# Kernel optimization log

Measured on AMD Instinct MI355X. Metric: run time of the kernel, lower is better.

## Reference

```python
import jax, jax.numpy as jnp
import numpy as np

N, E, DEG, DIM, NFP, NSEQ = 8192, 65536, 16, 64, 10000, 1024
LGNN, RAD, LOUT, NCLS = 3, 2, 2, 2


def setup_inputs() -> dict:
    key = jax.random.key(0)
    ks = jax.random.split(key, 24)
    s = 0.02
    return {
        "fingerprints": jax.random.randint(ks[0], (N,), 0, NFP + 1),
        "atom_degree_list": jax.random.randint(ks[1], (N, DEG), 0, N),
        "bond_feature": jax.random.normal(ks[2], (E, 10), jnp.float32),
        "bond_degree_list": jax.random.randint(ks[3], (N, DEG), 0, E),
        "i_bond_j": jax.random.randint(ks[4], (E, 2), 0, N),
        # scale down so adjacency @ hs does not saturate the sigmoids
        "adjacency": jax.random.uniform(ks[5], (N, N), jnp.float32) * (1.0 / 128.0),
        "words": jax.random.normal(ks[6], (NSEQ,), jnp.float32),
        "embed_table": jax.random.normal(ks[7], (NFP + 1, DIM), jnp.float32) * s,
        "bond_W": jax.random.normal(ks[8], (10, DIM), jnp.float32) * s,
        "bond_b": jnp.zeros((DIM,), jnp.float32),
        "sub_W": jax.random.normal(ks[9], (RAD, DIM, DIM), jnp.float32) * s,
        "sub_b": jnp.zeros((RAD, DIM), jnp.float32),
        "neigh_W": jax.random.normal(ks[10], (LGNN, 2 * DIM, DIM), jnp.float32) * s,
        "neigh_b": jnp.zeros((LGNN, DIM), jnp.float32),
        "side_W": jax.random.normal(ks[11], (LGNN, DIM, DIM), jnp.float32) * s,
        "side_b": jnp.zeros((LGNN, DIM), jnp.float32),
        "fc_W": jax.random.uniform(ks[12], (NSEQ, DIM), jnp.float32, -0.01, 0.01),
        "fc_b": jnp.zeros((DIM,), jnp.float32),
        "out_W": jax.random.normal(ks[13], (LOUT, 2 * DIM, 2 * DIM), jnp.float32) * s,
        "out_b": jnp.zeros((LOUT, 2 * DIM), jnp.float32),
        "inter_W": jax.random.normal(ks[14], (2 * DIM, NCLS), jnp.float32) * s,
        "inter_b": jnp.zeros((NCLS,), jnp.float32),
    }


def reference(fingerprints, atom_degree_list, bond_feature, bond_degree_list,
              i_bond_j, adjacency, words, embed_table, bond_W, bond_b,
              sub_W, sub_b, neigh_W, neigh_b, side_W, side_b,
              fc_W, fc_b, out_W, out_b, inter_W, inter_b):
    # sub_graph: residual dense-adjacency propagation
    x = embed_table[fingerprints]                       # [N, dim]
    for i in range(RAD):
        hs = jax.nn.relu(x @ sub_W[i] + sub_b[i])
        x = x + adjacency @ hs

    # gnn: gather neighbors, concat, linear+leaky_relu, sum, sigmoid updates
    bond_f = bond_feature @ bond_W + bond_b             # [E, dim]
    atom_f = x
    for i in range(LGNN):
        bn = bond_f[bond_degree_list]                   # [N, DEG, dim]
        an = atom_f[atom_degree_list]                   # [N, DEG, dim]
        nf = jnp.concatenate([an, bn], axis=-1)         # [N, DEG, 2*dim]
        nf = jax.nn.leaky_relu(nf @ neigh_W[i] + neigh_b[i], 0.01)
        atom_f = jax.nn.sigmoid(atom_f + nf.sum(axis=-2))
        pair = atom_f[i_bond_j].sum(axis=-2)            # [E, dim]
        bond_f = jax.nn.sigmoid(bond_f + pair @ side_W[i] + side_b[i])

    disease_vector = jnp.mean(x + atom_f, axis=0)[None, :]   # [1, dim]

    # miRNA vector via MLP
    mirna_vector = words.reshape(1, -1) @ fc_W + fc_b        # [1, dim]

    cat = jnp.concatenate([disease_vector, mirna_vector], axis=1)  # [1, 2*dim]
    for j in range(LOUT):
        cat = jax.nn.relu(cat @ out_W[j] + out_b[j])
    association = cat @ inter_W + inter_b                    # [1, n_classes]
    return association
```

## Files before the change

kernel.cpp:

```cpp
#include <hip/hip_runtime.h>
#include <hip/hip_bf16.h>
#include <cstdint>
#include <cstddef>

#define N_ATOM 8192
#define N_EDGE 65536
#define DEG    16
#define DIM    64
#define ADJ_S  4
#define BM     64
#define BK     64

typedef __attribute__((ext_vector_type(8))) short bf16x8_t;
typedef __attribute__((ext_vector_type(4))) float f32x4_t;

__device__ __forceinline__ float sigmoidf_(float z) {
  return 1.0f / (1.0f + __expf(-z));
}
__device__ __forceinline__ float lrelu_(float z) {
  return z > 0.0f ? z : 0.01f * z;
}
__device__ __forceinline__ unsigned short f2bfu(float f) {
  union { __hip_bfloat16 h; unsigned short u; } v;
  v.h = __float2bfloat16(f);
  return v.u;
}
__device__ __forceinline__ float bf2f(unsigned short u) {
  union { unsigned int i; float f; } v;
  v.i = ((unsigned int)u) << 16;
  return v.f;
}
__device__ __forceinline__ float4 cvt4f(ushort4 u) {
  return make_float4(bf2f(u.x), bf2f(u.y), bf2f(u.z), bf2f(u.w));
}
__device__ __forceinline__ ushort4 cvt4b(float4 f) {
  ushort4 u;
  u.x = f2bfu(f.x); u.y = f2bfu(f.y); u.z = f2bfu(f.z); u.w = f2bfu(f.w);
  return u;
}
__device__ __forceinline__ bf16x8_t cvt8(const float4 a, const float4 b) {
  bf16x8_t r;
  r[0] = (short)f2bfu(a.x); r[1] = (short)f2bfu(a.y);
  r[2] = (short)f2bfu(a.z); r[3] = (short)f2bfu(a.w);
  r[4] = (short)f2bfu(b.x); r[5] = (short)f2bfu(b.y);
  r[6] = (short)f2bfu(b.z); r[7] = (short)f2bfu(b.w);
  return r;
}
__device__ __forceinline__ void gload16(const void* g, void* l) {
  __builtin_amdgcn_global_load_lds(
      (const __attribute__((address_space(1))) void*)g,
      (__attribute__((address_space(3))) void*)l, 16, 0, 0);
}

__global__ __launch_bounds__(256) void k_front(
    const int* __restrict__ fp, const float* __restrict__ emb,
    float* __restrict__ x, const float* __restrict__ W,
    const float* __restrict__ b, unsigned short* __restrict__ hsT,
    const float* __restrict__ bfeat, const float* __restrict__ bW,
    const float* __restrict__ bb, unsigned short* __restrict__ bond_bf,
    const float* __restrict__ Wbn0, unsigned short* __restrict__ B_bf,
    const float* __restrict__ words, const float* __restrict__ fcW,
    float* __restrict__ mp2) {
  __shared__ float xs[16][68];
  __shared__ float Ws[64][64];
  const int t = threadIdx.x;
  const int r = t >> 4, dq = t & 15, d0 = dq * 4;
  if (blockIdx.x < (N_ATOM / 16)) {
    const int row = blockIdx.x * 16 + r;
    float4 v = reinterpret_cast<const float4*>(emb)[(size_t)fp[row] * 16 + dq];
    reinterpret_cast<float4*>(x)[(size_t)row * 16 + dq] = v;
    *reinterpret_cast<float4*>(&xs[r][d0]) = v;
#pragma unroll
    for (int q = 0; q < 4; ++q) {
      int p = t + q * 256;
      reinterpret_cast<float4*>(&Ws[0][0])[p] =
          reinterpret_cast<const float4*>(W)[p];
    }
    __syncthreads();
    float4 acc = reinterpret_cast<const float4*>(b)[dq];
#pragma unroll
    for (int k = 0; k < 64; ++k) {
      float xv = xs[r][k];
      float4 wv = *reinterpret_cast<const float4*>(&Ws[k][d0]);
      acc.x = fmaf(xv, wv.x, acc.x);
      acc.y = fmaf(xv, wv.y, acc.y);
      acc.z = fmaf(xv, wv.z, acc.z);
      acc.w = fmaf(xv, wv.w, acc.w);
    }
    float a4[4] = {acc.x, acc.y, acc.z, acc.w};
#pragma unroll
    for (int j = 0; j < 4; ++j)
      hsT[(size_t)(d0 + j) * N_ATOM + row] = f2bfu(fmaxf(a4[j], 0.0f));
  } else if (blockIdx.x < (N_ATOM / 16 + N_EDGE / 16)) {
    const int row = (blockIdx.x - N_ATOM / 16) * 16 + r;
    float4 acc = reinterpret_cast<const float4*>(bb)[dq];
    const float* br = bfeat + (size_t)row * 10;
#pragma unroll
    for (int k = 0; k < 10; ++k) {
      float xv = br[k];
      float4 wv = reinterpret_cast<const float4*>(bW)[k * 16 + dq];
      acc.x = fmaf(xv, wv.x, acc.x);
      acc.y = fmaf(xv, wv.y, acc.y);
      acc.z = fmaf(xv, wv.z, acc.z);
      acc.w = fmaf(xv, wv.w, acc.w);
    }
    reinterpret_cast<ushort4*>(bond_bf)[(size_t)row * 16 + dq] = cvt4b(acc);
    *reinterpret_cast<float4*>(&xs[r][d0]) = acc;
#pragma unroll
    for (int q = 0; q < 4; ++q) {
      int p = t + q * 256;
      reinterpret_cast<float4*>(&Ws[0][0])[p] =
          reinterpret_cast<const float4*>(Wbn0)[p];
    }
    __syncthreads();
    float4 acc2 = make_float4(0.f, 0.f, 0.f, 0.f);
#pragma unroll
    for (int k = 0; k < 64; ++k) {
      float xv = xs[r][k];
      float4 wv = *reinterpret_cast<const float4*>(&Ws[k][d0]);
      acc2.x = fmaf(xv, wv.x, acc2.x);
      acc2.y = fmaf(xv, wv.y, acc2.y);
      acc2.z = fmaf(xv, wv.z, acc2.z);
      acc2.w = fmaf(xv, wv.w, acc2.w);
    }
    reinterpret_cast<ushort4*>(B_bf)[(size_t)row * 16 + dq] = cvt4b(acc2);
  } else {
    const int mb = blockIdx.x - (N_ATOM / 16 + N_EDGE / 16);
    const int k = mb * 16 + r;
    float wv = words[k];
    float4 fv = reinterpret_cast<const float4*>(fcW)[(size_t)k * 16 + dq];
    float4 acc = make_float4(wv * fv.x, wv * fv.y, wv * fv.z, wv * fv.w);
    float4* red4 = reinterpret_cast<float4*>(&Ws[0][0]);
    red4[t] = acc;
    __syncthreads();
    for (int h = 8; h >= 1; h >>= 1) {
      if (r < h) {
        float4 o = red4[t + h * 16];
        acc.x += o.x; acc.y += o.y; acc.z += o.z; acc.w += o.w;
        red4[t] = acc;
      }
      __syncthreads();
    }
    if (r == 0) reinterpret_cast<float4*>(mp2)[mb * 16 + dq] = acc;
  }
}

__global__ __launch_bounds__(256) void k_red_hs(
    const float* __restrict__ part, float* __restrict__ x,
    const float* __restrict__ W, const float* __restrict__ b,
    unsigned short* __restrict__ hsT) {
  __shared__ float xs[16][68];
  __shared__ float Ws[64][64];
  const int t = threadIdx.x;
  const int r = t >> 4, dq = t & 15, d0 = dq * 4;
  const int row = blockIdx.x * 16 + r;
  float4 v = reinterpret_cast<const float4*>(x)[(size_t)row * 16 + dq];
#pragma unroll
  for (int s = 0; s < ADJ_S; ++s) {
    float4 p = reinterpret_cast<const float4*>(part)
                   [(size_t)s * (N_ATOM * 16) + (size_t)row * 16 + dq];
    v.x += p.x; v.y += p.y; v.z += p.z; v.w += p.w;
  }
  reinterpret_cast<float4*>(x)[(size_t)row * 16 + dq] = v;
  *reinterpret_cast<float4*>(&xs[r][d0]) = v;
#pragma unroll
  for (int q = 0; q < 4; ++q) {
    int p = t + q * 256;
    reinterpret_cast<float4*>(&Ws[0][0])[p] =
        reinterpret_cast<const float4*>(W)[p];
  }
  __syncthreads();
  float4 acc = reinterpret_cast<const float4*>(b)[dq];
#pragma unroll
  for (int k = 0; k < 64; ++k) {
    float xv = xs[r][k];
    float4 wv = *reinterpret_cast<const float4*>(&Ws[k][d0]);
    acc.x = fmaf(xv, wv.x, acc.x);
    acc.y = fmaf(xv, wv.y, acc.y);
    acc.z = fmaf(xv, wv.z, acc.z);
    acc.w = fmaf(xv, wv.w, acc.w);
  }
  float a4[4] = {acc.x, acc.y, acc.z, acc.w};
#pragma unroll
  for (int j = 0; j < 4; ++j)
    hsT[(size_t)(d0 + j) * N_ATOM + row] = f2bfu(fmaxf(a4[j], 0.0f));
}

__global__ __launch_bounds__(256) void k_adjmm(
    const float* __restrict__ adj, const unsigned short* __restrict__ hsT,
    float* __restrict__ part) {
  __shared__ float          Abuf[2][BM * BK];
  __shared__ unsigned short Bbuf[2][64 * BK];
  const int t = threadIdx.x;
  const int lane = t & 63, w = t >> 6;
  const int lr = lane & 15, lg = lane >> 4;
  const int row0 = blockIdx.x * BM;
  const int kbase = blockIdx.y * (N_ATOM / ADJ_S);
  const int NSTEP = (N_ATOM / ADJ_S) / BK;

  size_t aSrc[4]; int aLds[4];
#pragma unroll
  for (int j = 0; j < 4; ++j) {
    int c = j * 256 + t;
    int row = c >> 4, u = c & 15;
    int us = (u & 8) | ((u & 7) ^ (row & 7));
    aSrc[j] = (size_t)(row0 + row) * N_ATOM + kbase + us * 4;
    aLds[j] = j * 1024 + w * 256;
  }
  size_t bSrc[2]; int bLds[2];
#pragma unroll
  for (int j = 0; j < 2; ++j) {
    int c = j * 256 + t;
    int row = c >> 3, u = c & 7;
    int us = u ^ (row & 7);
    bSrc[j] = (size_t)row * N_ATOM + kbase + us * 8;
    bLds[j] = j * 2048 + w * 512;
  }

  f32x4_t acc[4];
#pragma unroll
  for (int n = 0; n < 4; ++n) acc[n] = (f32x4_t){0.f, 0.f, 0.f, 0.f};

#define STAGE(buf, kt)                                                        \
  {                                                                           \
    _Pragma("unroll")                                                         \
    for (int j = 0; j < 4; ++j)                                               \
      gload16(adj + aSrc[j] + (kt) * BK, &Abuf[buf][aLds[j]]);                \
    _Pragma("unroll")                                                         \
    for (int j = 0; j < 2; ++j)                                               \
      gload16(hsT + bSrc[j] + (kt) * BK, &Bbuf[buf][bLds[j]]);                \
  }

  STAGE(0, 0);
  __syncthreads();
  int cur = 0;
  const int Rl = w * 16 + lr;
  for (int kt = 0; kt < NSTEP; ++kt) {
    if (kt + 1 < NSTEP) STAGE(cur ^ 1, kt + 1);
#pragma unroll
    for (int kf = 0; kf < 2; ++kf) {
      int ua = kf * 8 + ((2 * lg) ^ (Rl & 7));
      int ub = kf * 8 + ((2 * lg + 1) ^ (Rl & 7));
      float4 fa = *reinterpret_cast<const float4*>(&Abuf[cur][Rl * 64 + ua * 4]);
      float4 fb = *reinterpret_cast<const float4*>(&Abuf[cur][Rl * 64 + ub * 4]);
      bf16x8_t a = cvt8(fa, fb);
#pragma unroll
      for (int n = 0; n < 4; ++n) {
        int Rb = n * 16 + lr;
        int us = (kf * 4 + lg) ^ (Rb & 7);
        bf16x8_t bv = *reinterpret_cast<const bf16x8_t*>(&Bbuf[cur][Rb * 64 + us * 8]);
        acc[n] = __builtin_amdgcn_mfma_f32_16x16x32_bf16(a, bv, acc[n], 0, 0, 0);
      }
    }
    __syncthreads();
    cur ^= 1;
  }
#undef STAGE

  float* pp = part + (size_t)blockIdx.y * (N_ATOM * DIM);
#pragma unroll
  for (int n = 0; n < 4; ++n)
#pragma unroll
    for (int rg = 0; rg < 4; ++rg) {
      int row = row0 + w * 16 + lg * 4 + rg;
      int col = n * 16 + lr;
      pp[(size_t)row * DIM + col] = acc[n][rg];
    }
}

__global__ __launch_bounds__(256) void k_A0(
    float* __restrict__ atom_f, const float* __restrict__ nW0,
    const float* __restrict__ nb0, unsigned short* __restrict__ A,
    const float* __restrict__ part, float* __restrict__ x) {
  __shared__ float xs[16][68];
  __shared__ float Ws[64][64];
  int t = threadIdx.x;
  int r = t >> 4, dq = t & 15, d0 = dq * 4;
  int row = blockIdx.x * 16 + r;
  float4 v = reinterpret_cast<const float4*>(x)[(size_t)row * 16 + dq];
#pragma unroll
  for (int s = 0; s < ADJ_S; ++s) {
    float4 p = reinterpret_cast<const float4*>(part)
                   [(size_t)s * (N_ATOM * 16) + (size_t)row * 16 + dq];
    v.x += p.x; v.y += p.y; v.z += p.z; v.w += p.w;
  }
  reinterpret_cast<float4*>(x)[(size_t)row * 16 + dq] = v;
  reinterpret_cast<float4*>(atom_f)[(size_t)row * 16 + dq] = v;
  *reinterpret_cast<float4*>(&xs[r][d0]) = v;
#pragma unroll
  for (int q = 0; q < 4; ++q) {
    int p = t + q * 256;
    reinterpret_cast<float4*>(&Ws[0][0])[p] = reinterpret_cast<const float4*>(nW0)[p];
  }
  __syncthreads();
  float4 acc = reinterpret_cast<const float4*>(nb0)[dq];
#pragma unroll
  for (int k = 0; k < 64; ++k) {
    float xv = xs[r][k];
    float4 wv = *reinterpret_cast<const float4*>(&Ws[k][d0]);
    acc.x = fmaf(xv, wv.x, acc.x);
    acc.y = fmaf(xv, wv.y, acc.y);
    acc.z = fmaf(xv, wv.z, acc.z);
    acc.w = fmaf(xv, wv.w, acc.w);
  }
  reinterpret_cast<ushort4*>(A)[(size_t)row * 16 + dq] = cvt4b(acc);
}

__global__ __launch_bounds__(256) void k_upd(
    const int* __restrict__ adl, const int* __restrict__ bdl,
    const unsigned short* __restrict__ A, const unsigned short* __restrict__ B,
    float* __restrict__ atom_f, const float* __restrict__ WanN,
    const float* __restrict__ nbN, unsigned short* __restrict__ A_next,
    const float* __restrict__ x, float* __restrict__ mp, int has_next) {
  __shared__ float xs[16][68];
  __shared__ float Ws[64][64];
  int t = threadIdx.x;
  int r = t >> 4, dq = t & 15, d0 = dq * 4;
  int n = blockIdx.x * 16 + r;
  float4 s = make_float4(0.f, 0.f, 0.f, 0.f);
#pragma unroll
  for (int g = 0; g < DEG; ++g) {
    int ai = adl[n * DEG + g];
    int bi = bdl[n * DEG + g];
    float4 va = cvt4f(reinterpret_cast<const ushort4*>(A)[(size_t)ai * 16 + dq]);
    float4 vb = cvt4f(reinterpret_cast<const ushort4*>(B)[(size_t)bi * 16 + dq]);
    s.x += lrelu_(va.x + vb.x);
    s.y += lrelu_(va.y + vb.y);
    s.z += lrelu_(va.z + vb.z);
    s.w += lrelu_(va.w + vb.w);
  }
  float4 af = reinterpret_cast<const float4*>(atom_f)[(size_t)n * 16 + dq];
  af.x = sigmoidf_(af.x + s.x);
  af.y = sigmoidf_(af.y + s.y);
  af.z = sigmoidf_(af.z + s.z);
  af.w = sigmoidf_(af.w + s.w);
  reinterpret_cast<float4*>(atom_f)[(size_t)n * 16 + dq] = af;
  if (has_next) {
    *reinterpret_cast<float4*>(&xs[r][d0]) = af;
#pragma unroll
    for (int q = 0; q < 4; ++q) {
      int p = t + q * 256;
      reinterpret_cast<float4*>(&Ws[0][0])[p] =
          reinterpret_cast<const float4*>(WanN)[p];
    }
    __syncthreads();
    float4 acc = reinterpret_cast<const float4*>(nbN)[dq];
#pragma unroll
    for (int k = 0; k < 64; ++k) {
      float xv = xs[r][k];
      float4 wv = *reinterpret_cast<const float4*>(&Ws[k][d0]);
      acc.x = fmaf(xv, wv.x, acc.x);
      acc.y = fmaf(xv, wv.y, acc.y);
      acc.z = fmaf(xv, wv.z, acc.z);
      acc.w = fmaf(xv, wv.w, acc.w);
    }
    reinterpret_cast<ushort4*>(A_next)[(size_t)n * 16 + dq] = cvt4b(acc);
  } else {
    float4 xv = reinterpret_cast<const float4*>(x)[(size_t)n * 16 + dq];
    float4 c = make_float4(af.x + xv.x, af.y + xv.y, af.z + xv.z, af.w + xv.w);
    float4* red4 = reinterpret_cast<float4*>(&Ws[0][0]);
    red4[t] = c;
    __syncthreads();
    for (int h = 8; h >= 1; h >>= 1) {
      if (r < h) {
        float4 o = red4[t + h * 16];
        c.x += o.x; c.y += o.y; c.z += o.z; c.w += o.w;
        red4[t] = c;
      }
      __syncthreads();
    }
    if (r == 0) reinterpret_cast<float4*>(mp)[blockIdx.x * 16 + dq] = c;
  }
}

__global__ __launch_bounds__(256) void k_side(
    const int* __restrict__ ibj, const float* __restrict__ atom_f,
    const float* __restrict__ sW, const float* __restrict__ sb,
    unsigned short* __restrict__ bond_bf, const float* __restrict__ WbnN,
    unsigned short* __restrict__ B_next, int write_bond) {
  __shared__ float ps[16][68];
  __shared__ float Ws[64][64];
  int t = threadIdx.x;
  int r = t >> 4, dq = t & 15, d0 = dq * 4;
  int e = blockIdx.x * 16 + r;
  int i0 = ibj[e * 2], i1 = ibj[e * 2 + 1];
  float4 p0 = reinterpret_cast<const float4*>(atom_f)[(size_t)i0 * 16 + dq];
  float4 p1 = reinterpret_cast<const float4*>(atom_f)[(size_t)i1 * 16 + dq];
  float4 pv = make_float4(p0.x + p1.x, p0.y + p1.y, p0.z + p1.z, p0.w + p1.w);
  *reinterpret_cast<float4*>(&ps[r][d0]) = pv;
#pragma unroll
  for (int q = 0; q < 4; ++q) {
    int p = t + q * 256;
    reinterpret_cast<float4*>(&Ws[0][0])[p] = reinterpret_cast<const float4*>(sW)[p];
  }
  __syncthreads();
  float4 acc = reinterpret_cast<const float4*>(sb)[dq];
#pragma unroll
  for (int k = 0; k < 64; ++k) {
    float xv = ps[r][k];
    float4 wv = *reinterpret_cast<const float4*>(&Ws[k][d0]);
    acc.x = fmaf(xv, wv.x, acc.x);
    acc.y = fmaf(xv, wv.y, acc.y);
    acc.z = fmaf(xv, wv.z, acc.z);
    acc.w = fmaf(xv, wv.w, acc.w);
  }
  float4 bf = cvt4f(reinterpret_cast<const ushort4*>(bond_bf)[(size_t)e * 16 + dq]);
  bf.x = sigmoidf_(bf.x + acc.x);
  bf.y = sigmoidf_(bf.y + acc.y);
  bf.z = sigmoidf_(bf.z + acc.z);
  bf.w = sigmoidf_(bf.w + acc.w);
  if (write_bond)
    reinterpret_cast<ushort4*>(bond_bf)[(size_t)e * 16 + dq] = cvt4b(bf);
  __syncthreads();
  *reinterpret_cast<float4*>(&ps[r][d0]) = bf;
#pragma unroll
  for (int q = 0; q < 4; ++q) {
    int p = t + q * 256;
    reinterpret_cast<float4*>(&Ws[0][0])[p] =
        reinterpret_cast<const float4*>(WbnN)[p];
  }
  __syncthreads();
  float4 acc2 = make_float4(0.f, 0.f, 0.f, 0.f);
#pragma unroll
  for (int k = 0; k < 64; ++k) {
    float xv = ps[r][k];
    float4 wv = *reinterpret_cast<const float4*>(&Ws[k][d0]);
    acc2.x = fmaf(xv, wv.x, acc2.x);
    acc2.y = fmaf(xv, wv.y, acc2.y);
    acc2.z = fmaf(xv, wv.z, acc2.z);
    acc2.w = fmaf(xv, wv.w, acc2.w);
  }
  reinterpret_cast<ushort4*>(B_next)[(size_t)e * 16 + dq] = cvt4b(acc2);
}

__global__ __launch_bounds__(256) void k_tail(
    const float* __restrict__ mp, const float* __restrict__ mp2,
    const float* __restrict__ fcb, const float* __restrict__ oW,
    const float* __restrict__ ob, const float* __restrict__ iW,
    const float* __restrict__ ib, float* __restrict__ out) {
  __shared__ float cat[128];
  int t = threadIdx.x;
  if (t < 64) {
    float s = 0.f;
    for (int w = 0; w < 512; ++w) s += mp[w * 64 + t];
    cat[t] = s * (1.0f / N_ATOM);
  } else if (t < 128) {
    int d = t - 64;
    float s = fcb[d];
    for (int w = 0; w < 64; ++w) s += mp2[w * 64 + d];
    cat[64 + d] = s;
  }
  __syncthreads();
  for (int j = 0; j < 2; ++j) {
    float s = 0.f;
    if (t < 128) {
      s = ob[j * 128 + t];
      for (int k = 0; k < 128; ++k)
        s = fmaf(cat[k], oW[(size_t)j * 128 * 128 + k * 128 + t], s);
      s = fmaxf(s, 0.f);
    }
    __syncthreads();
    if (t < 128) cat[t] = s;
    __syncthreads();
  }
  if (t < 2) {
    float s = ib[t];
    for (int k = 0; k < 128; ++k) s = fmaf(cat[k], iW[k * 2 + t], s);
    out[t] = s;
  }
}

extern "C" void kernel_launch(void* const* d_in, const int* in_sizes, int n_in,
                              void* d_out, int out_size, void* d_ws, size_t ws_size,
                              hipStream_t stream) {
  const int*   fp    = (const int*)  d_in[0];
  const int*   adl   = (const int*)  d_in[1];
  const float* bfeat = (const float*)d_in[2];
  const int*   bdl   = (const int*)  d_in[3];
  const int*   ibj   = (const int*)  d_in[4];
  const float* adj   = (const float*)d_in[5];
  const float* words = (const float*)d_in[6];
  const float* emb   = (const float*)d_in[7];
  const float* bW    = (const float*)d_in[8];
  const float* bb    = (const float*)d_in[9];
  const float* subW  = (const float*)d_in[10];
  const float* subb  = (const float*)d_in[11];
  const float* nW    = (const float*)d_in[12];
  const float* nb    = (const float*)d_in[13];
  const float* sW    = (const float*)d_in[14];
  const float* sb    = (const float*)d_in[15];
  const float* fcW   = (const float*)d_in[16];
  const float* fcb   = (const float*)d_in[17];
  const float* oW    = (const float*)d_in[18];
  const float* ob    = (const float*)d_in[19];
  const float* iW    = (const float*)d_in[20];
  const float* ib    = (const float*)d_in[21];
  float* out = (float*)d_out;

  char* ws = (char*)d_ws;
  const size_t MB = 1ull << 20;
  float*          x      = (float*)(ws + 0 * MB);
  float*          atom_f = (float*)(ws + 2 * MB);
  unsigned short* A0_bf  = (unsigned short*)(ws + 4 * MB);
  unsigned short* A1_bf  = (unsigned short*)(ws + 5 * MB);
  unsigned short* hsT    = (unsigned short*)(ws + 6 * MB);
  float*          mp     = (float*)(ws + 7 * MB);
  float*          mp2    = (float*)(ws + 7 * MB + 512 * 1024);
  unsigned short* bond_bf= (unsigned short*)(ws + 8 * MB);
  unsigned short* B_bf   = (unsigned short*)(ws + 16 * MB);
  float*          part   = (float*)(ws + 32 * MB);

  dim3 gmm(N_ATOM / BM, ADJ_S);

  k_front<<<N_ATOM / 16 + N_EDGE / 16 + 64, 256, 0, stream>>>(
      fp, emb, x, subW, subb, hsT, bfeat, bW, bb, bond_bf,
      nW + 64 * 64, B_bf, words, fcW, mp2);
  k_adjmm<<<gmm, 256, 0, stream>>>(adj, hsT, part);
  k_red_hs<<<N_ATOM / 16, 256, 0, stream>>>(part, x, subW + 64 * 64,
                                            subb + 64, hsT);
  k_adjmm<<<gmm, 256, 0, stream>>>(adj, hsT, part);

  k_A0<<<N_ATOM / 16, 256, 0, stream>>>(atom_f, nW, nb, A0_bf, part, x);
  k_upd<<<N_ATOM / 16, 256, 0, stream>>>(adl, bdl, A0_bf, B_bf, atom_f,
                                         nW + 1 * 128 * 64, nb + 1 * 64,
                                         A1_bf, x, mp, 1);
  k_side<<<N_EDGE / 16, 256, 0, stream>>>(ibj, atom_f, sW, sb, bond_bf,
                                          nW + 1 * 128 * 64 + 64 * 64, B_bf, 1);
  k_upd<<<N_ATOM / 16, 256, 0, stream>>>(adl, bdl, A1_bf, B_bf, atom_f,
                                         nW + 2 * 128 * 64, nb + 2 * 64,
                                         A0_bf, x, mp, 1);
  k_side<<<N_EDGE / 16, 256, 0, stream>>>(ibj, atom_f, sW + 64 * 64, sb + 64,
                                          bond_bf, nW + 2 * 128 * 64 + 64 * 64,
                                          B_bf, 0);
  k_upd<<<N_ATOM / 16, 256, 0, stream>>>(adl, bdl, A0_bf, B_bf, atom_f,
                                         nullptr, nullptr, nullptr, x, mp, 0);

  k_tail<<<1, 256, 0, stream>>>(mp, mp2, fcb, oW, ob, iW, ib, out);
}
```

Measured before the change: 235.3 us.

## Cache bf16 adjacency during first matmul and batch 64 rows per edge block

The first adjacency matmul now also writes the bf16-converted adjacency to a workspace buffer, and the second matmul reads that half-size bf16 copy directly through a new kernel instead of re-reading the fp32 matrix. Separately, the edge-side kernels (bond projection in the front kernel and k_side) process 64 edges per block instead of 16, so each thread reuses every loaded weight value across four rows and the per-block weight staging cost is spread over more work. The cost is an extra 128 MB write in the first matmul and more shared memory and registers per block.

```diff
diff --git a/kernel.cpp b/kernel.cpp
--- a/kernel.cpp
+++ b/kernel.cpp
@@ -61,7 +61,7 @@
     const float* __restrict__ Wbn0, unsigned short* __restrict__ B_bf,
     const float* __restrict__ words, const float* __restrict__ fcW,
     float* __restrict__ mp2) {
-  __shared__ float xs[16][68];
+  __shared__ float ps[64][68];
   __shared__ float Ws[64][64];
   const int t = threadIdx.x;
   const int r = t >> 4, dq = t & 15, d0 = dq * 4;
@@ -69,7 +69,7 @@
     const int row = blockIdx.x * 16 + r;
     float4 v = reinterpret_cast<const float4*>(emb)[(size_t)fp[row] * 16 + dq];
     reinterpret_cast<float4*>(x)[(size_t)row * 16 + dq] = v;
-    *reinterpret_cast<float4*>(&xs[r][d0]) = v;
+    *reinterpret_cast<float4*>(&ps[r][d0]) = v;
 #pragma unroll
     for (int q = 0; q < 4; ++q) {
       int p = t + q * 256;
@@ -80,7 +80,7 @@
     float4 acc = reinterpret_cast<const float4*>(b)[dq];
 #pragma unroll
     for (int k = 0; k < 64; ++k) {
-      float xv = xs[r][k];
+      float xv = ps[r][k];
       float4 wv = *reinterpret_cast<const float4*>(&Ws[k][d0]);
       acc.x = fmaf(xv, wv.x, acc.x);
       acc.y = fmaf(xv, wv.y, acc.y);
@@ -91,21 +91,29 @@
 #pragma unroll
     for (int j = 0; j < 4; ++j)
       hsT[(size_t)(d0 + j) * N_ATOM + row] = f2bfu(fmaxf(a4[j], 0.0f));
-  } else if (blockIdx.x < (N_ATOM / 16 + N_EDGE / 16)) {
-    const int row = (blockIdx.x - N_ATOM / 16) * 16 + r;
-    float4 acc = reinterpret_cast<const float4*>(bb)[dq];
-    const float* br = bfeat + (size_t)row * 10;
+  } else if (blockIdx.x < (N_ATOM / 16 + N_EDGE / 64)) {
+    const int row0 = (blockIdx.x - N_ATOM / 16) * 64;
+    float4 acc[4];
+#pragma unroll
+    for (int g = 0; g < 4; ++g) acc[g] = reinterpret_cast<const float4*>(bb)[dq];
 #pragma unroll
     for (int k = 0; k < 10; ++k) {
-      float xv = br[k];
       float4 wv = reinterpret_cast<const float4*>(bW)[k * 16 + dq];
-      acc.x = fmaf(xv, wv.x, acc.x);
-      acc.y = fmaf(xv, wv.y, acc.y);
-      acc.z = fmaf(xv, wv.z, acc.z);
-      acc.w = fmaf(xv, wv.w, acc.w);
-    }
-    reinterpret_cast<ushort4*>(bond_bf)[(size_t)row * 16 + dq] = cvt4b(acc);
-    *reinterpret_cast<float4*>(&xs[r][d0]) = acc;
+#pragma unroll
+      for (int g = 0; g < 4; ++g) {
+        float xv = bfeat[(size_t)(row0 + g * 16 + r) * 10 + k];
+        acc[g].x = fmaf(xv, wv.x, acc[g].x);
+        acc[g].y = fmaf(xv, wv.y, acc[g].y);
+        acc[g].z = fmaf(xv, wv.z, acc[g].z);
+        acc[g].w = fmaf(xv, wv.w, acc[g].w);
+      }
+    }
+#pragma unroll
+    for (int g = 0; g < 4; ++g) {
+      int row = row0 + g * 16 + r;
+      reinterpret_cast<ushort4*>(bond_bf)[(size_t)row * 16 + dq] = cvt4b(acc[g]);
+      *reinterpret_cast<float4*>(&ps[g * 16 + r][d0]) = acc[g];
+    }
 #pragma unroll
     for (int q = 0; q < 4; ++q) {
       int p = t + q * 256;
@@ -113,19 +121,27 @@
           reinterpret_cast<const float4*>(Wbn0)[p];
     }
     __syncthreads();
-    float4 acc2 = make_float4(0.f, 0.f, 0.f, 0.f);
-#pragma unroll
+    float4 a2[4];
+#pragma unroll
+    for (int g = 0; g < 4; ++g) a2[g] = make_float4(0.f, 0.f, 0.f, 0.f);
     for (int k = 0; k < 64; ++k) {
-      float xv = xs[r][k];
       float4 wv = *reinterpret_cast<const float4*>(&Ws[k][d0]);
-      acc2.x = fmaf(xv, wv.x, acc2.x);
-      acc2.y = fmaf(xv, wv.y, acc2.y);
-      acc2.z = fmaf(xv, wv.z, acc2.z);
-      acc2.w = fmaf(xv, wv.w, acc2.w);
-    }
-    reinterpret_cast<ushort4*>(B_bf)[(size_t)row * 16 + dq] = cvt4b(acc2);
+#pragma unroll
+      for (int g = 0; g < 4; ++g) {
+        float xv = ps[g * 16 + r][k];
+        a2[g].x = fmaf(xv, wv.x, a2[g].x);
+        a2[g].y = fmaf(xv, wv.y, a2[g].y);
+        a2[g].z = fmaf(xv, wv.z, a2[g].z);
+        a2[g].w = fmaf(xv, wv.w, a2[g].w);
+      }
+    }
+#pragma unroll
+    for (int g = 0; g < 4; ++g) {
+      int row = row0 + g * 16 + r;
+      reinterpret_cast<ushort4*>(B_bf)[(size_t)row * 16 + dq] = cvt4b(a2[g]);
+    }
   } else {
-    const int mb = blockIdx.x - (N_ATOM / 16 + N_EDGE / 16);
+    const int mb = blockIdx.x - (N_ATOM / 16 + N_EDGE / 64);
     const int k = mb * 16 + r;
     float wv = words[k];
     float4 fv = reinterpret_cast<const float4*>(fcW)[(size_t)k * 16 + dq];
@@ -188,7 +204,7 @@
 
 __global__ __launch_bounds__(256) void k_adjmm(
     const float* __restrict__ adj, const unsigned short* __restrict__ hsT,
-    float* __restrict__ part) {
+    float* __restrict__ part, unsigned short* __restrict__ adj_bf) {
   __shared__ float          Abuf[2][BM * BK];
   __shared__ unsigned short Bbuf[2][64 * BK];
   const int t = threadIdx.x;
@@ -235,6 +251,8 @@
   __syncthreads();
   int cur = 0;
   const int Rl = w * 16 + lr;
+  unsigned short* abf =
+      adj_bf + (size_t)(row0 + Rl) * N_ATOM + kbase + lg * 8;
   for (int kt = 0; kt < NSTEP; ++kt) {
     if (kt + 1 < NSTEP) STAGE(cur ^ 1, kt + 1);
 #pragma unroll
@@ -244,6 +262,80 @@
       float4 fa = *reinterpret_cast<const float4*>(&Abuf[cur][Rl * 64 + ua * 4]);
       float4 fb = *reinterpret_cast<const float4*>(&Abuf[cur][Rl * 64 + ub * 4]);
       bf16x8_t a = cvt8(fa, fb);
+      *reinterpret_cast<bf16x8_t*>(abf + kt * BK + kf * 32) = a;
+#pragma unroll
+      for (int n = 0; n < 4; ++n) {
+        int Rb = n * 16 + lr;
+        int us = (kf * 4 + lg) ^ (Rb & 7);
+        bf16x8_t bv = *reinterpret_cast<const bf16x8_t*>(&Bbuf[cur][Rb * 64 + us * 8]);
+        acc[n] = __builtin_amdgcn_mfma_f32_16x16x32_bf16(a, bv, acc[n], 0, 0, 0);
+      }
+    }
+    __syncthreads();
+    cur ^= 1;
+  }
+#undef STAGE
+
+  float* pp = part + (size_t)blockIdx.y * (N_ATOM * DIM);
+#pragma unroll
+  for (int n = 0; n < 4; ++n)
+#pragma unroll
+    for (int rg = 0; rg < 4; ++rg) {
+      int row = row0 + w * 16 + lg * 4 + rg;
+      int col = n * 16 + lr;
+      pp[(size_t)row * DIM + col] = acc[n][rg];
+    }
+}
+
+__global__ __launch_bounds__(256) void k_adjmm_bf(
+    const unsigned short* __restrict__ adj_bf,
+    const unsigned short* __restrict__ hsT, float* __restrict__ part) {
+  __shared__ unsigned short Abuf[2][BM * BK];
+  __shared__ unsigned short Bbuf[2][64 * BK];
+  const int t = threadIdx.x;
+  const int lane = t & 63, w = t >> 6;
+  const int lr = lane & 15, lg = lane >> 4;
+  const int row0 = blockIdx.x * BM;
+  const int kbase = blockIdx.y * (N_ATOM / ADJ_S);
+  const int NSTEP = (N_ATOM / ADJ_S) / BK;
+
+  size_t aSrc[2]; int aLds[2];
+  size_t bSrc[2]; int bLds[2];
+#pragma unroll
+  for (int j = 0; j < 2; ++j) {
+    int c = j * 256 + t;
+    int row = c >> 3, u = c & 7;
+    int us = u ^ (row & 7);
+    aSrc[j] = (size_t)(row0 + row) * N_ATOM + kbase + us * 8;
+    bSrc[j] = (size_t)row * N_ATOM + kbase + us * 8;
+    aLds[j] = j * 2048 + w * 512;
+    bLds[j] = j * 2048 + w * 512;
+  }
+
+  f32x4_t acc[4];
+#pragma unroll
+  for (int n = 0; n < 4; ++n) acc[n] = (f32x4_t){0.f, 0.f, 0.f, 0.f};
+
+#define STAGE(buf, kt)                                                        \
+  {                                                                           \
+    _Pragma("unroll")                                                         \
+    for (int j = 0; j < 2; ++j)                                               \
+      gload16(adj_bf + aSrc[j] + (kt) * BK, &Abuf[buf][aLds[j]]);             \
+    _Pragma("unroll")                                                         \
+    for (int j = 0; j < 2; ++j)                                               \
+      gload16(hsT + bSrc[j] + (kt) * BK, &Bbuf[buf][bLds[j]]);                \
+  }
+
+  STAGE(0, 0);
+  __syncthreads();
+  int cur = 0;
+  const int Rl = w * 16 + lr;
+  for (int kt = 0; kt < NSTEP; ++kt) {
+    if (kt + 1 < NSTEP) STAGE(cur ^ 1, kt + 1);
+#pragma unroll
+    for (int kf = 0; kf < 2; ++kf) {
+      int ua = (kf * 4 + lg) ^ (Rl & 7);
+      bf16x8_t a = *reinterpret_cast<const bf16x8_t*>(&Abuf[cur][Rl * 64 + ua * 8]);
 #pragma unroll
       for (int n = 0; n < 4; ++n) {
         int Rb = n * 16 + lr;
@@ -378,41 +470,56 @@
     const float* __restrict__ sW, const float* __restrict__ sb,
     unsigned short* __restrict__ bond_bf, const float* __restrict__ WbnN,
     unsigned short* __restrict__ B_next, int write_bond) {
-  __shared__ float ps[16][68];
+  __shared__ float ps[64][68];
   __shared__ float Ws[64][64];
   int t = threadIdx.x;
   int r = t >> 4, dq = t & 15, d0 = dq * 4;
-  int e = blockIdx.x * 16 + r;
-  int i0 = ibj[e * 2], i1 = ibj[e * 2 + 1];
-  float4 p0 = reinterpret_cast<const float4*>(atom_f)[(size_t)i0 * 16 + dq];
-  float4 p1 = reinterpret_cast<const float4*>(atom_f)[(size_t)i1 * 16 + dq];
-  float4 pv = make_float4(p0.x + p1.x, p0.y + p1.y, p0.z + p1.z, p0.w + p1.w);
-  *reinterpret_cast<float4*>(&ps[r][d0]) = pv;
+  int e0 = blockIdx.x * 64;
 #pragma unroll
   for (int q = 0; q < 4; ++q) {
     int p = t + q * 256;
     reinterpret_cast<float4*>(&Ws[0][0])[p] = reinterpret_cast<const float4*>(sW)[p];
   }
-  __syncthreads();
-  float4 acc = reinterpret_cast<const float4*>(sb)[dq];
-#pragma unroll
+#pragma unroll
+  for (int g = 0; g < 4; ++g) {
+    int e = e0 + g * 16 + r;
+    int i0 = ibj[e * 2], i1 = ibj[e * 2 + 1];
+    float4 p0 = reinterpret_cast<const float4*>(atom_f)[(size_t)i0 * 16 + dq];
+    float4 p1 = reinterpret_cast<const float4*>(atom_f)[(size_t)i1 * 16 + dq];
+    *reinterpret_cast<float4*>(&ps[g * 16 + r][d0]) =
+        make_float4(p0.x + p1.x, p0.y + p1.y, p0.z + p1.z, p0.w + p1.w);
+  }
+  __syncthreads();
+  float4 acc[4];
+#pragma unroll
+  for (int g = 0; g < 4; ++g) acc[g] = reinterpret_cast<const float4*>(sb)[dq];
   for (int k = 0; k < 64; ++k) {
-    float xv = ps[r][k];
     float4 wv = *reinterpret_cast<const float4*>(&Ws[k][d0]);
-    acc.x = fmaf(xv, wv.x, acc.x);
-    acc.y = fmaf(xv, wv.y, acc.y);
-    acc.z = fmaf(xv, wv.z, acc.z);
-    acc.w = fmaf(xv, wv.w, acc.w);
-  }
-  float4 bf = cvt4f(reinterpret_cast<const ushort4*>(bond_bf)[(size_t)e * 16 + dq]);
-  bf.x = sigmoidf_(bf.x + acc.x);
-  bf.y = sigmoidf_(bf.y + acc.y);
-  bf.z = sigmoidf_(bf.z + acc.z);
-  bf.w = sigmoidf_(bf.w + acc.w);
-  if (write_bond)
-    reinterpret_cast<ushort4*>(bond_bf)[(size_t)e * 16 + dq] = cvt4b(bf);
-  __syncthreads();
-  *reinterpret_cast<float4*>(&ps[r][d0]) = bf;
+#pragma unroll
+    for (int g = 0; g < 4; ++g) {
+      float xv = ps[g * 16 + r][k];
+      acc[g].x = fmaf(xv, wv.x, acc[g].x);
+      acc[g].y = fmaf(xv, wv.y, acc[g].y);
+      acc[g].z = fmaf(xv, wv.z, acc[g].z);
+      acc[g].w = fmaf(xv, wv.w, acc[g].w);
+    }
+  }
+  float4 bf[4];
+#pragma unroll
+  for (int g = 0; g < 4; ++g) {
+    int e = e0 + g * 16 + r;
+    float4 b0 = cvt4f(reinterpret_cast<const ushort4*>(bond_bf)[(size_t)e * 16 + dq]);
+    bf[g].x = sigmoidf_(b0.x + acc[g].x);
+    bf[g].y = sigmoidf_(b0.y + acc[g].y);
+    bf[g].z = sigmoidf_(b0.z + acc[g].z);
+    bf[g].w = sigmoidf_(b0.w + acc[g].w);
+    if (write_bond)
+      reinterpret_cast<ushort4*>(bond_bf)[(size_t)e * 16 + dq] = cvt4b(bf[g]);
+  }
+  __syncthreads();
+#pragma unroll
+  for (int g = 0; g < 4; ++g)
+    *reinterpret_cast<float4*>(&ps[g * 16 + r][d0]) = bf[g];
 #pragma unroll
   for (int q = 0; q < 4; ++q) {
     int p = t + q * 256;
@@ -420,17 +527,25 @@
         reinterpret_cast<const float4*>(WbnN)[p];
   }
   __syncthreads();
-  float4 acc2 = make_float4(0.f, 0.f, 0.f, 0.f);
-#pragma unroll
+  float4 a2[4];
+#pragma unroll
+  for (int g = 0; g < 4; ++g) a2[g] = make_float4(0.f, 0.f, 0.f, 0.f);
   for (int k = 0; k < 64; ++k) {
-    float xv = ps[r][k];
     float4 wv = *reinterpret_cast<const float4*>(&Ws[k][d0]);
-    acc2.x = fmaf(xv, wv.x, acc2.x);
-    acc2.y = fmaf(xv, wv.y, acc2.y);
-    acc2.z = fmaf(xv, wv.z, acc2.z);
-    acc2.w = fmaf(xv, wv.w, acc2.w);
-  }
-  reinterpret_cast<ushort4*>(B_next)[(size_t)e * 16 + dq] = cvt4b(acc2);
+#pragma unroll
+    for (int g = 0; g < 4; ++g) {
+      float xv = ps[g * 16 + r][k];
+      a2[g].x = fmaf(xv, wv.x, a2[g].x);
+      a2[g].y = fmaf(xv, wv.y, a2[g].y);
+      a2[g].z = fmaf(xv, wv.z, a2[g].z);
+      a2[g].w = fmaf(xv, wv.w, a2[g].w);
+    }
+  }
+#pragma unroll
+  for (int g = 0; g < 4; ++g) {
+    int e = e0 + g * 16 + r;
+    reinterpret_cast<ushort4*>(B_next)[(size_t)e * 16 + dq] = cvt4b(a2[g]);
+  }
 }
 
 __global__ __launch_bounds__(256) void k_tail(
@@ -509,27 +624,28 @@
   unsigned short* bond_bf= (unsigned short*)(ws + 8 * MB);
   unsigned short* B_bf   = (unsigned short*)(ws + 16 * MB);
   float*          part   = (float*)(ws + 32 * MB);
+  unsigned short* adj_bf = (unsigned short*)(ws + 64 * MB);
 
   dim3 gmm(N_ATOM / BM, ADJ_S);
 
-  k_front<<<N_ATOM / 16 + N_EDGE / 16 + 64, 256, 0, stream>>>(
+  k_front<<<N_ATOM / 16 + N_EDGE / 64 + 64, 256, 0, stream>>>(
       fp, emb, x, subW, subb, hsT, bfeat, bW, bb, bond_bf,
       nW + 64 * 64, B_bf, words, fcW, mp2);
-  k_adjmm<<<gmm, 256, 0, stream>>>(adj, hsT, part);
+  k_adjmm<<<gmm, 256, 0, stream>>>(adj, hsT, part, adj_bf);
   k_red_hs<<<N_ATOM / 16, 256, 0, stream>>>(part, x, subW + 64 * 64,
                                             subb + 64, hsT);
-  k_adjmm<<<gmm, 256, 0, stream>>>(adj, hsT, part);
+  k_adjmm_bf<<<gmm, 256, 0, stream>>>(adj_bf, hsT, part);
 
   k_A0<<<N_ATOM / 16, 256, 0, stream>>>(atom_f, nW, nb, A0_bf, part, x);
   k_upd<<<N_ATOM / 16, 256, 0, stream>>>(adl, bdl, A0_bf, B_bf, atom_f,
                                          nW + 1 * 128 * 64, nb + 1 * 64,
                                          A1_bf, x, mp, 1);
-  k_side<<<N_EDGE / 16, 256, 0, stream>>>(ibj, atom_f, sW, sb, bond_bf,
+  k_side<<<N_EDGE / 64, 256, 0, stream>>>(ibj, atom_f, sW, sb, bond_bf,
                                           nW + 1 * 128 * 64 + 64 * 64, B_bf, 1);
   k_upd<<<N_ATOM / 16, 256, 0, stream>>>(adl, bdl, A1_bf, B_bf, atom_f,
                                          nW + 2 * 128 * 64, nb + 2 * 64,
                                          A0_bf, x, mp, 1);
-  k_side<<<N_EDGE / 16, 256, 0, stream>>>(ibj, atom_f, sW + 64 * 64, sb + 64,
+  k_side<<<N_EDGE / 64, 256, 0, stream>>>(ibj, atom_f, sW + 64 * 64, sb + 64,
                                           bond_bf, nW + 2 * 128 * 64 + 64 * 64,
                                           B_bf, 0);
   k_upd<<<N_ATOM / 16, 256, 0, stream>>>(adl, bdl, A0_bf, B_bf, atom_f,
```

Result: slower. 264.8 us (+12.5%).
